# Optimization experiments

Measured on AMD Instinct MI355X. Metric: run time of the kernel, lower is better.

Reference implementation:

```python
import jax, jax.numpy as jnp
import numpy as np

_FRAC_BITS = 8  # assumed fixed-point fractional bits for bits_quant
_SCALE = float(2 ** _FRAC_BITS)

def bits_quant(x):
    # Simulated fixed-point quantization: round to nearest multiple of 2^-8.
    return jnp.round(x * _SCALE) / _SCALE


def setup_inputs() -> dict:
    key = jax.random.key(0)
    k1, k2, k3 = jax.random.split(key, 3)
    B, D_in, D_out = 4096, 4096, 4096
    inputs = jax.random.normal(k1, (B, D_in), dtype=jnp.float32)
    w = jax.random.normal(k2, (D_in, D_out), dtype=jnp.float32) * 0.02
    b = jax.random.normal(k3, (D_out,), dtype=jnp.float32) * 0.02
    return {"inputs": inputs, "w": w, "b": b}


def reference(inputs, w, b):
    # y = bits_quant(inputs @ w) + bits_quant(b); out = bits_quant(y)
    y = bits_quant(jnp.matmul(inputs, w)) + bits_quant(b)
    return bits_quant(y)
```

## Files before the change

### kernel.cpp

```cpp
#include <hip/hip_runtime.h>
#include <math.h>

typedef __attribute__((ext_vector_type(8)))  short  short8;
typedef __attribute__((ext_vector_type(16))) float  f32x16;
typedef __attribute__((ext_vector_type(4)))  float  float4v;
typedef __attribute__((ext_vector_type(8)))  unsigned short ushort8;
typedef __attribute__((ext_vector_type(4)))  unsigned short ushort4v;

#define NDIM 4096
#define BM 256
#define BN 256
#define BK 64
#define T_TILES (NDIM / BK)
#define HALF_USH 8192
#define B_BASE   (5 * HALF_USH)

#define NA_BLOCKS 2048
#define NW_BLOCKS 4096

__device__ __forceinline__ unsigned short f2bf(float f) {
  unsigned u = __builtin_bit_cast(unsigned, f);
  u += 0x7fffu + ((u >> 16) & 1u);
  return (unsigned short)(u >> 16);
}

__device__ __forceinline__ void gload_lds16(const unsigned short* g, unsigned short* l) {
  __builtin_amdgcn_global_load_lds(
      (const __attribute__((address_space(1))) void*)g,
      (__attribute__((address_space(3))) void*)l, 16, 0, 0);
}

__global__ __launch_bounds__(256)
void prep(const float* __restrict__ A, unsigned short* __restrict__ Abf,
          const float* __restrict__ W, unsigned short* __restrict__ Wt) {
  __shared__ unsigned short tile[64][72];
  const int t = threadIdx.x;
  if (blockIdx.x < NA_BLOCKS) {
    const int base   = blockIdx.x * 256 + t;
    const int stride = NA_BLOCKS * 256;
#pragma unroll
    for (int it = 0; it < 8; ++it) {
      const size_t idx = (size_t)(base + it * stride) * 4;
      float4v v = *(const float4v*)(A + idx);
      ushort4v o;
      o[0] = f2bf(v[0]); o[1] = f2bf(v[1]); o[2] = f2bf(v[2]); o[3] = f2bf(v[3]);
      *(ushort4v*)(Abf + idx) = o;
    }
  } else {
    const int b  = blockIdx.x - NA_BLOCKS;
    const int n0 = (b & 63) * 64;
    const int k0 = (b >> 6) * 64;
    const int kq = t >> 4;
    const int nc = (t & 15) * 4;
    float4v v[4];
#pragma unroll
    for (int r = 0; r < 4; ++r)
      v[r] = *(const float4v*)&W[(size_t)(k0 + kq * 4 + r) * NDIM + n0 + nc];
#pragma unroll
    for (int c = 0; c < 4; ++c) {
      ushort4v u;
#pragma unroll
      for (int r = 0; r < 4; ++r) u[r] = f2bf(v[r][c]);
      *(ushort4v*)&tile[nc + c][kq * 4] = u;
    }
    __syncthreads();
    const int n  = t >> 2;
    const int cb = (t & 3) * 16;
    unsigned short* dst = Wt + (size_t)(n0 + n) * NDIM + k0 + cb;
#pragma unroll
    for (int h = 0; h < 2; ++h) {
      ushort8 w8 = *(const ushort8*)&tile[n][cb + h * 8];
      *(ushort8*)(dst + h * 8) = w8;
    }
  }
}

__global__ __launch_bounds__(512, 2)
void gemm_bt_quant(const unsigned short* __restrict__ A,
                   const unsigned short* __restrict__ Bt,
                   const float* __restrict__ bias,
                   float* __restrict__ C) {
  __shared__ unsigned short lds[9 * HALF_USH];

  const int tid  = threadIdx.x;
  const int lane = tid & 63;
  const int wid  = tid >> 6;
  const int wr   = wid >> 2;
  const int wc   = wid & 3;
  const int hb   = wc >> 1;
  const int bnr  = (wc & 1) * 64;

  const int bid  = blockIdx.y * 16 + blockIdx.x;
  const int swz  = (bid & 7) * 32 + (bid >> 3);
  const int m0   = (swz >> 4) * BM;
  const int n0   = (swz & 15) * BN;

  const int srow = tid >> 3;
  const int sc   = (tid & 7) ^ (srow & 7);
  const unsigned short* Ag = A  + (size_t)(m0 + srow) * NDIM + sc * 8;
  const unsigned short* Bg = Bt + (size_t)(n0 + srow) * NDIM + sc * 8;

  const int fr  = lane & 31;
  const int fh  = lane >> 5;
  const int fsw = fr & 7;

  auto stageA = [&](int tt, int ha, int slot) {
    unsigned short* dst = &lds[slot * HALF_USH];
    const unsigned short* g = Ag + (size_t)(ha * 128) * NDIM + tt * 64;
    gload_lds16(g,                       &dst[tid * 8]);
    gload_lds16(g + (size_t)64 * NDIM,   &dst[(512 + tid) * 8]);
  };
  auto stageB = [&](int tt, int hb2, int slot) {
    unsigned short* dst = &lds[B_BASE + slot * HALF_USH];
    const unsigned short* g = Bg + (size_t)(hb2 * 128) * NDIM + tt * 64;
    gload_lds16(g,                       &dst[tid * 8]);
    gload_lds16(g + (size_t)64 * NDIM,   &dst[(512 + tid) * 8]);
  };

  f32x16 acc[4][2] = {};

  stageB(0, 0, 0);
  stageB(0, 1, 1);
  stageA(0, 0, 0);
  stageA(0, 1, 1);
  stageB(1, 0, 2);
  stageB(1, 1, 3);

  int raA = wr;
  int rbB = hb;
  int sA0 = 2, sA1 = 3;
  int sB0 = 0, sB1 = 1;

  for (int t = 0; t < T_TILES; ++t) {
    const unsigned short* Ah = &lds[raA * HALF_USH];
    const unsigned short* Bh = &lds[B_BASE + rbB * HALF_USH];
    short8 bk[2][4];
#pragma unroll
    for (int p = 0; p < 4; ++p) {
      if (p == 0) {
        if (t < T_TILES - 1) asm volatile("s_waitcnt vmcnt(4)" ::: "memory");
        else                 asm volatile("s_waitcnt vmcnt(0)" ::: "memory");
      }
      __builtin_amdgcn_s_barrier();
      __builtin_amdgcn_sched_barrier(0);

      if (p == 0) {
#pragma unroll
        for (int j = 0; j < 2; ++j)
#pragma unroll
          for (int h = 0; h < 4; ++h)
            bk[j][h] = *(const short8*)&Bh[(bnr + j * 32 + fr) * 64 + ((2 * h + fh) ^ fsw) * 8];
      }
      short8 af[4];
#pragma unroll
      for (int h = 0; h < 4; ++h)
        af[h] = *(const short8*)&Ah[(p * 32 + fr) * 64 + ((2 * h + fh) ^ fsw) * 8];

      if (p == 0 && t + 1 < T_TILES) stageA(t + 1, 0, sA0);
      if (p == 1 && t + 1 < T_TILES) stageA(t + 1, 1, sA1);
      if (p == 2 && t + 2 < T_TILES) stageB(t + 2, 0, sB0);
      if (p == 3 && t + 2 < T_TILES) stageB(t + 2, 1, sB1);

      asm volatile("s_waitcnt lgkmcnt(0)" ::: "memory");
      __builtin_amdgcn_sched_barrier(0);
      __builtin_amdgcn_s_setprio(1);
#pragma unroll
      for (int h = 0; h < 4; ++h)
#pragma unroll
        for (int j = 0; j < 2; ++j)
          acc[p][j] = __builtin_amdgcn_mfma_f32_32x32x16_bf16(af[h], bk[j][h], acc[p][j], 0, 0, 0);
      __builtin_amdgcn_s_setprio(0);
    }
    raA += 2; if (raA >= 5) raA -= 5;
    sA0 += 2; if (sA0 >= 5) sA0 -= 5;
    sA1 += 2; if (sA1 >= 5) sA1 -= 5;
    rbB = (rbB + 2) & 3;
    sB0 = (sB0 + 2) & 3;
    sB1 = (sB1 + 2) & 3;
  }

  const float inv = 1.0f / 256.0f;
#pragma unroll
  for (int j = 0; j < 2; ++j) {
    const int col = n0 + wc * 64 + j * 32 + fr;
    const float qb = rintf(bias[col] * 256.0f) * inv;
#pragma unroll
    for (int p = 0; p < 4; ++p) {
      const int rb = m0 + wr * 128 + p * 32 + 4 * fh;
#pragma unroll
      for (int r = 0; r < 16; ++r) {
        const int row = rb + (r & 3) + 8 * (r >> 2);
        C[(size_t)row * NDIM + col] = rintf(acc[p][j][r] * 256.0f) * inv + qb;
      }
    }
  }
}

__global__ void gemm_fb(const float* __restrict__ A, const float* __restrict__ W,
                        const float* __restrict__ bias, float* __restrict__ C) {
  __shared__ float As[32][33], Ws[32][33];
  int tx = threadIdx.x, ty = threadIdx.y;
  int m0 = blockIdx.y * 32, n0 = blockIdx.x * 32;
  float acc[4] = {0.f, 0.f, 0.f, 0.f};
  for (int k0 = 0; k0 < NDIM; k0 += 32) {
#pragma unroll
    for (int i = 0; i < 4; ++i) {
      int r = ty + i * 8;
      As[r][tx] = A[(size_t)(m0 + r) * NDIM + k0 + tx];
      Ws[r][tx] = W[(size_t)(k0 + r) * NDIM + n0 + tx];
    }
    __syncthreads();
#pragma unroll
    for (int k = 0; k < 32; ++k) {
      float wv = Ws[k][tx];
#pragma unroll
      for (int i = 0; i < 4; ++i) acc[i] += As[ty + i * 8][k] * wv;
    }
    __syncthreads();
  }
  float qb = rintf(bias[n0 + tx] * 256.0f) * (1.0f / 256.0f);
#pragma unroll
  for (int i = 0; i < 4; ++i)
    C[(size_t)(m0 + ty + i * 8) * NDIM + n0 + tx] =
        rintf(acc[i] * 256.0f) * (1.0f / 256.0f) + qb;
}

extern "C" void kernel_launch(void* const* d_in, const int* in_sizes, int n_in,
                              void* d_out, int out_size, void* d_ws, size_t ws_size,
                              hipStream_t stream) {
  const float* A    = (const float*)d_in[0];
  const float* W    = (const float*)d_in[1];
  const float* bias = (const float*)d_in[2];
  float* C = (float*)d_out;
  const size_t nElem = (size_t)NDIM * NDIM;

  if (ws_size >= nElem * 4) {
    unsigned short* Abf = (unsigned short*)d_ws;
    unsigned short* Wt  = Abf + nElem;
    prep<<<NA_BLOCKS + NW_BLOCKS, 256, 0, stream>>>(A, Abf, W, Wt);
    gemm_bt_quant<<<dim3(16, 16), 512, 0, stream>>>(Abf, Wt, bias, C);
  } else {
    gemm_fb<<<dim3(128, 128), dim3(32, 8), 0, stream>>>(A, W, bias, C);
  }
}
```

Measured before the change: 298.4 us.

## Pre-tile bf16 operands into MFMA fragment images for contiguous LDS staging

The prep kernel now writes A and W in bf16 as per-tile images already laid out in MFMA fragment order. The GEMM can then stage each tile with contiguous global-to-LDS copies and read fragments at lane-linear offsets, with no XOR swizzle or row-strided gathers. The LDS ring becomes a simpler double buffer, with an extra barrier after each MFMA phase and launch bounds lowered to one block per CU. The goal is less address arithmetic and better coalescing, at the cost of more synchronisation and possibly lower occupancy or overlap.

```diff
diff --git a/kernel.cpp b/kernel.cpp
--- a/kernel.cpp
+++ b/kernel.cpp
@@ -12,11 +12,7 @@
 #define BN 256
 #define BK 64
 #define T_TILES (NDIM / BK)
-#define HALF_USH 8192
-#define B_BASE   (5 * HALF_USH)
-
-#define NA_BLOCKS 2048
-#define NW_BLOCKS 4096
+#define IMG_USH 8192
 
 __device__ __forceinline__ unsigned short f2bf(float f) {
   unsigned u = __builtin_bit_cast(unsigned, f);
@@ -33,54 +29,52 @@
 __global__ __launch_bounds__(256)
 void prep(const float* __restrict__ A, unsigned short* __restrict__ Abf,
           const float* __restrict__ W, unsigned short* __restrict__ Wt) {
-  __shared__ unsigned short tile[64][72];
   const int t = threadIdx.x;
-  if (blockIdx.x < NA_BLOCKS) {
-    const int base   = blockIdx.x * 256 + t;
-    const int stride = NA_BLOCKS * 256;
-#pragma unroll
-    for (int it = 0; it < 8; ++it) {
-      const size_t idx = (size_t)(base + it * stride) * 4;
-      float4v v = *(const float4v*)(A + idx);
-      ushort4v o;
-      o[0] = f2bf(v[0]); o[1] = f2bf(v[1]); o[2] = f2bf(v[2]); o[3] = f2bf(v[3]);
-      *(ushort4v*)(Abf + idx) = o;
+  if (blockIdx.x < 2048) {
+    const int b  = blockIdx.x;
+    const int mb = b >> 6, kt = b & 63;
+    const int h  = (t >> 6) & 3, fh = (t >> 5) & 1, fr = t & 31;
+    const float* src0 = A + (size_t)(mb * 128 + fr) * NDIM + kt * 64 + h * 16 + fh * 8;
+    unsigned short* dst = Abf + ((size_t)(mb * 64 + kt) * 1024 + t) * 8;
+#pragma unroll
+    for (int p = 0; p < 4; ++p) {
+      const float* s = src0 + (size_t)(p * 32) * NDIM;
+      float4v a = *(const float4v*)s;
+      float4v c = *(const float4v*)(s + 4);
+      ushort8 o;
+      o[0] = f2bf(a[0]); o[1] = f2bf(a[1]); o[2] = f2bf(a[2]); o[3] = f2bf(a[3]);
+      o[4] = f2bf(c[0]); o[5] = f2bf(c[1]); o[6] = f2bf(c[2]); o[7] = f2bf(c[3]);
+      *(ushort8*)(dst + (size_t)p * 2048) = o;
     }
   } else {
-    const int b  = blockIdx.x - NA_BLOCKS;
-    const int n0 = (b & 63) * 64;
-    const int k0 = (b >> 6) * 64;
-    const int kq = t >> 4;
-    const int nc = (t & 15) * 4;
-    float4v v[4];
-#pragma unroll
-    for (int r = 0; r < 4; ++r)
-      v[r] = *(const float4v*)&W[(size_t)(k0 + kq * 4 + r) * NDIM + n0 + nc];
+    const int b  = blockIdx.x - 2048;
+    const int nb = b >> 6, kt = b & 63;
+    const int n0 = (t & 31) * 4;
+    const int kq = t >> 5;
+    float4v v[8];
+#pragma unroll
+    for (int r = 0; r < 8; ++r)
+      v[r] = *(const float4v*)&W[(size_t)(kt * 64 + kq * 8 + r) * NDIM + nb * 128 + n0];
+    const int q  = (t & 31) >> 3;
+    const int h  = kq >> 1, fh = kq & 1;
+    unsigned short* img = Wt + (size_t)(nb * 64 + kt) * IMG_USH;
 #pragma unroll
     for (int c = 0; c < 4; ++c) {
-      ushort4v u;
-#pragma unroll
-      for (int r = 0; r < 4; ++r) u[r] = f2bf(v[r][c]);
-      *(ushort4v*)&tile[nc + c][kq * 4] = u;
-    }
-    __syncthreads();
-    const int n  = t >> 2;
-    const int cb = (t & 3) * 16;
-    unsigned short* dst = Wt + (size_t)(n0 + n) * NDIM + k0 + cb;
-#pragma unroll
-    for (int h = 0; h < 2; ++h) {
-      ushort8 w8 = *(const ushort8*)&tile[n][cb + h * 8];
-      *(ushort8*)(dst + h * 8) = w8;
-    }
-  }
-}
-
-__global__ __launch_bounds__(512, 2)
-void gemm_bt_quant(const unsigned short* __restrict__ A,
-                   const unsigned short* __restrict__ Bt,
+      const int fr = (n0 + c) & 31;
+      ushort8 o;
+#pragma unroll
+      for (int r = 0; r < 8; ++r) o[r] = f2bf(v[r][c]);
+      *(ushort8*)(img + ((size_t)((q * 4 + h) * 64 + fh * 32 + fr)) * 8) = o;
+    }
+  }
+}
+
+__global__ __launch_bounds__(512, 1)
+void gemm_bt_quant(const unsigned short* __restrict__ Abf,
+                   const unsigned short* __restrict__ Wt,
                    const float* __restrict__ bias,
                    float* __restrict__ C) {
-  __shared__ unsigned short lds[9 * HALF_USH];
+  __shared__ unsigned short lds[8 * IMG_USH];
 
   const int tid  = threadIdx.x;
   const int lane = tid & 63;
@@ -88,79 +82,69 @@
   const int wr   = wid >> 2;
   const int wc   = wid & 3;
   const int hb   = wc >> 1;
-  const int bnr  = (wc & 1) * 64;
 
   const int bid  = blockIdx.y * 16 + blockIdx.x;
   const int swz  = (bid & 7) * 32 + (bid >> 3);
   const int m0   = (swz >> 4) * BM;
   const int n0   = (swz & 15) * BN;
-
-  const int srow = tid >> 3;
-  const int sc   = (tid & 7) ^ (srow & 7);
-  const unsigned short* Ag = A  + (size_t)(m0 + srow) * NDIM + sc * 8;
-  const unsigned short* Bg = Bt + (size_t)(n0 + srow) * NDIM + sc * 8;
-
-  const int fr  = lane & 31;
-  const int fh  = lane >> 5;
-  const int fsw = fr & 7;
-
-  auto stageA = [&](int tt, int ha, int slot) {
-    unsigned short* dst = &lds[slot * HALF_USH];
-    const unsigned short* g = Ag + (size_t)(ha * 128) * NDIM + tt * 64;
-    gload_lds16(g,                       &dst[tid * 8]);
-    gload_lds16(g + (size_t)64 * NDIM,   &dst[(512 + tid) * 8]);
+  const int mb0  = (swz >> 4) * 2;
+  const int nb0  = (swz & 15) * 2;
+
+  const unsigned short* Aimg = Abf + (size_t)mb0 * 64 * IMG_USH;
+  const unsigned short* Bimg = Wt  + (size_t)nb0 * 64 * IMG_USH;
+
+  auto stageA = [&](int u, int ha) {
+    unsigned short* dst = &lds[(ha * 2 + (u & 1)) * IMG_USH];
+    const unsigned short* src = Aimg + ((size_t)(ha * 64 + u)) * IMG_USH + tid * 8;
+    gload_lds16(src,        dst + tid * 8);
+    gload_lds16(src + 4096, dst + 4096 + tid * 8);
   };
-  auto stageB = [&](int tt, int hb2, int slot) {
-    unsigned short* dst = &lds[B_BASE + slot * HALF_USH];
-    const unsigned short* g = Bg + (size_t)(hb2 * 128) * NDIM + tt * 64;
-    gload_lds16(g,                       &dst[tid * 8]);
-    gload_lds16(g + (size_t)64 * NDIM,   &dst[(512 + tid) * 8]);
+  auto stageB = [&](int u, int h2) {
+    unsigned short* dst = &lds[(4 + h2 * 2 + (u & 1)) * IMG_USH];
+    const unsigned short* src = Bimg + ((size_t)(h2 * 64 + u)) * IMG_USH + tid * 8;
+    gload_lds16(src,        dst + tid * 8);
+    gload_lds16(src + 4096, dst + 4096 + tid * 8);
   };
 
   f32x16 acc[4][2] = {};
 
-  stageB(0, 0, 0);
-  stageB(0, 1, 1);
-  stageA(0, 0, 0);
-  stageA(0, 1, 1);
-  stageB(1, 0, 2);
-  stageB(1, 1, 3);
-
-  int raA = wr;
-  int rbB = hb;
-  int sA0 = 2, sA1 = 3;
-  int sB0 = 0, sB1 = 1;
-
-  for (int t = 0; t < T_TILES; ++t) {
-    const unsigned short* Ah = &lds[raA * HALF_USH];
-    const unsigned short* Bh = &lds[B_BASE + rbB * HALF_USH];
+  stageB(0, 0); stageB(0, 1);
+  stageA(0, 0); stageA(0, 1);
+  stageB(1, 0); stageB(1, 1);
+  asm volatile("s_waitcnt vmcnt(4)" ::: "memory");
+  __builtin_amdgcn_s_barrier();
+
+  const int lofs = lane * 8;
+
+  for (int u = 0; u < T_TILES; ++u) {
+    const unsigned short* Ah = &lds[(wr * 2 + (u & 1)) * IMG_USH];
+    const unsigned short* Bh = &lds[(4 + hb * 2 + (u & 1)) * IMG_USH + (wc & 1) * 4096];
     short8 bk[2][4];
 #pragma unroll
     for (int p = 0; p < 4; ++p) {
       if (p == 0) {
-        if (t < T_TILES - 1) asm volatile("s_waitcnt vmcnt(4)" ::: "memory");
+#pragma unroll
+        for (int j = 0; j < 2; ++j)
+#pragma unroll
+          for (int h = 0; h < 4; ++h)
+            bk[j][h] = *(const short8*)&Bh[j * 2048 + h * 512 + lofs];
+      }
+      short8 af[4];
+#pragma unroll
+      for (int h = 0; h < 4; ++h)
+        af[h] = *(const short8*)&Ah[p * 2048 + h * 512 + lofs];
+
+      if (p == 0 && u + 1 < T_TILES) stageA(u + 1, 0);
+      if (p == 1 && u + 1 < T_TILES) stageA(u + 1, 1);
+      if (p == 2 && u + 2 < T_TILES) stageB(u + 2, 0);
+      if (p == 3 && u + 2 < T_TILES) stageB(u + 2, 1);
+
+      __builtin_amdgcn_sched_barrier(0);
+      if (p == 3) {
+        if (u < T_TILES - 2) asm volatile("s_waitcnt vmcnt(4)" ::: "memory");
         else                 asm volatile("s_waitcnt vmcnt(0)" ::: "memory");
       }
       __builtin_amdgcn_s_barrier();
-      __builtin_amdgcn_sched_barrier(0);
-
-      if (p == 0) {
-#pragma unroll
-        for (int j = 0; j < 2; ++j)
-#pragma unroll
-          for (int h = 0; h < 4; ++h)
-            bk[j][h] = *(const short8*)&Bh[(bnr + j * 32 + fr) * 64 + ((2 * h + fh) ^ fsw) * 8];
-      }
-      short8 af[4];
-#pragma unroll
-      for (int h = 0; h < 4; ++h)
-        af[h] = *(const short8*)&Ah[(p * 32 + fr) * 64 + ((2 * h + fh) ^ fsw) * 8];
-
-      if (p == 0 && t + 1 < T_TILES) stageA(t + 1, 0, sA0);
-      if (p == 1 && t + 1 < T_TILES) stageA(t + 1, 1, sA1);
-      if (p == 2 && t + 2 < T_TILES) stageB(t + 2, 0, sB0);
-      if (p == 3 && t + 2 < T_TILES) stageB(t + 2, 1, sB1);
-
       asm volatile("s_waitcnt lgkmcnt(0)" ::: "memory");
       __builtin_amdgcn_sched_barrier(0);
       __builtin_amdgcn_s_setprio(1);
@@ -170,15 +154,13 @@
         for (int j = 0; j < 2; ++j)
           acc[p][j] = __builtin_amdgcn_mfma_f32_32x32x16_bf16(af[h], bk[j][h], acc[p][j], 0, 0, 0);
       __builtin_amdgcn_s_setprio(0);
-    }
-    raA += 2; if (raA >= 5) raA -= 5;
-    sA0 += 2; if (sA0 >= 5) sA0 -= 5;
-    sA1 += 2; if (sA1 >= 5) sA1 -= 5;
-    rbB = (rbB + 2) & 3;
-    sB0 = (sB0 + 2) & 3;
-    sB1 = (sB1 + 2) & 3;
-  }
-
+      __builtin_amdgcn_s_barrier();
+      __builtin_amdgcn_sched_barrier(0);
+    }
+  }
+
+  const int fr = lane & 31;
+  const int fh = lane >> 5;
   const float inv = 1.0f / 256.0f;
 #pragma unroll
   for (int j = 0; j < 2; ++j) {
@@ -237,7 +219,7 @@
   if (ws_size >= nElem * 4) {
     unsigned short* Abf = (unsigned short*)d_ws;
     unsigned short* Wt  = Abf + nElem;
-    prep<<<NA_BLOCKS + NW_BLOCKS, 256, 0, stream>>>(A, Abf, W, Wt);
+    prep<<<4096, 256, 0, stream>>>(A, Abf, W, Wt);
     gemm_bt_quant<<<dim3(16, 16), 512, 0, stream>>>(Abf, Wt, bias, C);
   } else {
     gemm_fb<<<dim3(128, 128), dim3(32, 8), 0, stream>>>(A, W, bias, C);
```

Measured after the change: 295.9 us. No clear change (-0.8%).
